# Kernel optimization log

Hardware: AMD Instinct MI355X
Metric: run time of the kernel (lower is better)

## Reference

```python
import jax, jax.numpy as jnp
import numpy as np

B, L, D_IN = 2048, 512, 32
PRED_LEN = 96
COND = 128      # cond_dim (z_dim)
XPROJ = 128     # x_proj_dim defaults to cond_dim
ODE_H = 128     # ode_hidden
TDIM = 128      # time_dim
HID = 256       # hidden of final MLP
N_STEPS = 32    # fixed-step RK4 steps over t in [0,1] (stands in for adaptive dopri5)
LN_EPS = 1e-5


def _linear(x, w, b):
    return x @ w.T + b


def _layernorm(x, g, b):
    mu = jnp.mean(x, axis=-1, keepdims=True)
    var = jnp.var(x, axis=-1, keepdims=True)
    return (x - mu) * jax.lax.rsqrt(var + LN_EPS) * g + b


def _interp(x_seq, t):
    # linear interp over sequence dim: x_seq (B,L,D), scalar t in [0,1] -> (B,D)
    Ls = x_seq.shape[1]
    pos = jnp.clip(t, 0.0, 1.0) * (Ls - 1)
    i0 = jnp.clip(jnp.floor(pos).astype(jnp.int32), 0, Ls - 1)
    i1 = jnp.clip(i0 + 1, 0, Ls - 1)
    w = (pos - i0.astype(pos.dtype))
    x0 = jax.lax.dynamic_index_in_dim(x_seq, i0, axis=1, keepdims=False)
    x1 = jax.lax.dynamic_index_in_dim(x_seq, i1, axis=1, keepdims=False)
    return (1.0 - w) * x0 + w * x1


def setup_inputs() -> dict:
    key = jax.random.key(0)
    ks = jax.random.split(key, 16)

    def kaiming(k, shape):
        return jax.random.normal(k, shape, jnp.float32) * np.float32(np.sqrt(2.0 / shape[-1]))

    IN_F = PRED_LEN * D_IN + COND + TDIM   # 3328
    OUT_F = PRED_LEN * D_IN                # 3072
    return {
        "x_t": jax.random.normal(ks[0], (B, PRED_LEN, D_IN), jnp.float32),
        "past": jax.random.normal(ks[1], (B, L, D_IN), jnp.float32),
        "t": jax.random.randint(ks[2], (B,), 0, 1000),
        "xproj_w": kaiming(ks[3], (XPROJ, D_IN)), "xproj_b": jnp.zeros((XPROJ,), jnp.float32),
        "z0_w": kaiming(ks[4], (COND, XPROJ)), "z0_b": jnp.zeros((COND,), jnp.float32),
        "ln_g": jnp.ones((COND,), jnp.float32), "ln_b": jnp.zeros((COND,), jnp.float32),
        "w1": kaiming(ks[5], (ODE_H, COND + XPROJ)), "b1": jnp.zeros((ODE_H,), jnp.float32),
        "w2": kaiming(ks[6], (ODE_H, ODE_H)), "b2": jnp.zeros((ODE_H,), jnp.float32),
        "w3": kaiming(ks[7], (COND, ODE_H)), "b3": jnp.zeros((COND,), jnp.float32),
        "fw1": kaiming(ks[8], (HID, IN_F)), "fb1": jnp.zeros((HID,), jnp.float32),
        "fw2": kaiming(ks[9], (HID, HID)), "fb2": jnp.zeros((HID,), jnp.float32),
        "fw3": kaiming(ks[10], (OUT_F, HID)), "fb3": jnp.zeros((OUT_F,), jnp.float32),
    }


def _time_emb(t):
    half = TDIM // 2
    freqs = jnp.exp(-np.float32(np.log(10000.0)) * jnp.arange(half, dtype=jnp.float32) / (half - 1))
    args = t.astype(jnp.float32)[:, None] * freqs[None, :]
    return jnp.concatenate([jnp.sin(args), jnp.cos(args)], axis=1)  # (B, TDIM)


def _forward(x_t, past, t, xproj_w, xproj_b, z0_w, z0_b, ln_g, ln_b,
             w1, b1, w2, b2, w3, b3, fw1, fb1, fw2, fb2, fw3, fb3):
    Bn = x_t.shape[0]
    x_seq = _linear(past, xproj_w, xproj_b)           # (B,L,XPROJ)
    z0 = _linear(x_seq[:, 0, :], z0_w, z0_b)          # (B,COND)

    def odef(tt, z):
        xt = _interp(x_seq, tt)                       # (B,XPROJ)
        zn = _layernorm(z, ln_g, ln_b)
        h = jnp.concatenate([zn, xt], axis=-1)
        h = jax.nn.silu(_linear(h, w1, b1))
        h = jax.nn.silu(_linear(h, w2, b2))
        return _linear(h, w3, b3)                     # (B,COND)

    dt = jnp.float32(1.0 / N_STEPS)

    def step(z, tt):
        k1 = odef(tt, z)
        k2 = odef(tt + dt * 0.5, z + dt * 0.5 * k1)
        k3 = odef(tt + dt * 0.5, z + dt * 0.5 * k2)
        k4 = odef(tt + dt, z + dt * k3)
        return z + (dt / 6.0) * (k1 + 2.0 * k2 + 2.0 * k3 + k4), None

    ts = jnp.arange(N_STEPS, dtype=jnp.float32) * dt
    cond, _ = jax.lax.scan(step, z0, ts)              # zT (B,COND)

    temb = _time_emb(t)                               # (B,TDIM)
    x_flat = x_t.reshape(Bn, -1)                      # (B,PRED_LEN*D_IN)
    h = jnp.concatenate([x_flat, cond, temb], axis=1)
    h = jax.nn.silu(_linear(h, fw1, fb1))
    h = jax.nn.silu(_linear(h, fw2, fb2))
    eps = _linear(h, fw3, fb3)
    return eps.reshape(Bn, PRED_LEN, D_IN)


def reference(x_t, past, t, xproj_w, xproj_b, z0_w, z0_b, ln_g, ln_b,
              w1, b1, w2, b2, w3, b3, fw1, fb1, fw2, fb2, fw3, fb3):
    return _forward(x_t, past, t, xproj_w, xproj_b, z0_w, z0_b, ln_g, ln_b,
                    w1, b1, w2, b2, w3, b3, fw1, fb1, fw2, fb2, fw3, fb3)
```

## Files before the change

### kernel.cpp

```cpp
#include <hip/hip_runtime.h>
#include <math.h>

typedef _Float16 h8f16 __attribute__((ext_vector_type(8)));
typedef _Float16 h2f16 __attribute__((ext_vector_type(2)));
typedef float f32x4 __attribute__((ext_vector_type(4)));

#define MFMA16(a, b, c) __builtin_amdgcn_mfma_f32_16x16x32_f16((a), (b), (c), 0, 0, 0)

__device__ __forceinline__ float silu_f(float v) {
    return v * __builtin_amdgcn_rcpf(1.0f + __expf(-v));
}

__device__ __forceinline__ void bar_lds() {
    asm volatile("s_waitcnt lgkmcnt(0)" ::: "memory");
    __builtin_amdgcn_s_barrier();
    __builtin_amdgcn_sched_barrier(0);
}

__global__ __launch_bounds__(512, 1) void ode_kernel(
    const float* __restrict__ past,
    const float* __restrict__ xproj_w, const float* __restrict__ xproj_b,
    const float* __restrict__ z0_w, const float* __restrict__ z0_b,
    const float* __restrict__ ln_g, const float* __restrict__ ln_b,
    const float* __restrict__ w1, const float* __restrict__ b1,
    const float* __restrict__ w2, const float* __restrict__ b2,
    const float* __restrict__ w3, const float* __restrict__ b3,
    float* __restrict__ zbuf)
{
    __shared__ _Float16 hbuf[16][136];
    __shared__ _Float16 h1S[16][136];
    __shared__ _Float16 h2S[16][136];
    __shared__ float    pS[16][33];
    __shared__ float    x0S[16][128];
    __shared__ float    zS0[16][129];

    const int tid  = threadIdx.x;
    const int wid  = tid >> 6;
    const int lane = tid & 63;
    const int lrow = lane & 15;
    const int lhi  = lane >> 4;
    const int b0   = blockIdx.x * 16;
    const int nc   = wid * 16 + lrow;
    const int koff = lhi * 8;

    h8f16 w1f[4], wcf, w2f[4], w3f[4];
    float b1t, b2r, b3r;
    {
#pragma unroll
        for (int ks = 0; ks < 4; ++ks) {
            h8f16 v1, v2, v3;
#pragma unroll
            for (int j = 0; j < 8; ++j) {
                const int k = ks * 32 + koff + j;
                v1[j] = (_Float16)(w1[nc * 256 + k] * ln_g[k]);
                v2[j] = (_Float16)w2[nc * 128 + k];
                v3[j] = (_Float16)w3[nc * 128 + k];
            }
            w1f[ks] = v1; w2f[ks] = v2; w3f[ks] = v3;
        }
        float wc[8] = {0, 0, 0, 0, 0, 0, 0, 0};
        float bc = 0.0f, bb = 0.0f;
        const float* w1a = w1 + nc * 256;
        const float* w1b = w1a + 128;
#pragma unroll 4
        for (int k = 0; k < 128; ++k) {
            const float a = w1b[k];
            bc += a * xproj_b[k];
            bb += w1a[k] * ln_b[k];
            const float* xr = xproj_w + k * 32 + koff;
#pragma unroll
            for (int j = 0; j < 8; ++j) wc[j] += a * xr[j];
        }
        h8f16 v;
#pragma unroll
        for (int j = 0; j < 8; ++j) v[j] = (_Float16)wc[j];
        wcf = v;
        b1t = b1[nc] + bc + bb;
        b2r = b2[nc]; b3r = b3[nc];
    }

    pS[tid >> 5][tid & 31] = past[(long)(b0 + (tid >> 5)) * 16384 + (tid & 31)];
    __syncthreads();
    {
        const int r  = tid >> 5;
        const int c0 = (tid & 31) * 4;
#pragma unroll
        for (int cc = 0; cc < 4; ++cc) {
            const int kc = c0 + cc;
            float s = xproj_b[kc];
            const float* xr = xproj_w + kc * 32;
#pragma unroll
            for (int c = 0; c < 32; ++c) s += pS[r][c] * xr[c];
            x0S[r][kc] = s;
        }
    }
    __syncthreads();
    {
        const int nn = tid & 127;
        const int r0 = (tid >> 7) * 4;
        for (int p = 0; p < 4; ++p) {
            const int r = r0 + p;
            float s = z0_b[nn];
            const float* zr = z0_w + nn * 128;
            for (int k = 0; k < 128; ++k) s += x0S[r][k] * zr[k];
            zS0[r][nn] = s;
        }
    }
    __syncthreads();

    float zc[4], krk[4];
#pragma unroll
    for (int j = 0; j < 4; ++j) {
        zc[j] = zS0[4 * lhi + j][nc];
        hbuf[4 * lhi + j][nc] = (_Float16)zc[j];
    }

    const float DT = 1.0f / 32.0f;

    f32x4 s0a, s0b, s1a, s1b;
    auto stage = [&](int e) {
        const float pos = (float)e * 7.984375f;
        const int i0 = (int)pos;
        const int i1 = (i0 < 511) ? i0 + 1 : 511;
        const float* base = past + (long)(b0 + lrow) * 16384;
        const float* p0 = base + i0 * 32 + koff;
        const float* p1 = base + i1 * 32 + koff;
        s0a = *(const f32x4*)p0; s0b = *(const f32x4*)(p0 + 4);
        s1a = *(const f32x4*)p1; s1b = *(const f32x4*)(p1 + 4);
    };
    auto blend = [&](int e) -> h8f16 {
        const float pos = (float)e * 7.984375f;
        const float w = pos - floorf(pos);
        h8f16 r;
#pragma unroll
        for (int j = 0; j < 4; ++j) {
            r[j]     = (_Float16)(s0a[j] + w * (s1a[j] - s0a[j]));
            r[4 + j] = (_Float16)(s0b[j] + w * (s1b[j] - s0b[j]));
        }
        return r;
    };

    const h2f16 one2 = {(_Float16)1.0f, (_Float16)1.0f};

    auto phaseA = [&](h8f16 bxc) {
        h8f16 xf[4];
#pragma unroll
        for (int ks = 0; ks < 4; ++ks)
            xf[ks] = *(const h8f16*)&hbuf[lrow][ks * 32 + koff];
        float s0 = 0.f, s1 = 0.f, q0 = 0.f, q1 = 0.f;
#pragma unroll
        for (int ks = 0; ks < 4; ++ks) {
#pragma unroll
            for (int p = 0; p < 4; ++p) {
                const h2f16 x2 = {xf[ks][2 * p], xf[ks][2 * p + 1]};
                if (p & 1) {
                    s1 = __builtin_amdgcn_fdot2(x2, one2, s1, false);
                    q1 = __builtin_amdgcn_fdot2(x2, x2, q1, false);
                } else {
                    s0 = __builtin_amdgcn_fdot2(x2, one2, s0, false);
                    q0 = __builtin_amdgcn_fdot2(x2, x2, q0, false);
                }
            }
        }
        float s = s0 + s1, q = q0 + q1;
        s += __shfl_xor(s, 16); q += __shfl_xor(q, 16);
        s += __shfl_xor(s, 32); q += __shfl_xor(q, 32);
        const float mu  = s * (1.0f / 128.0f);
        const float var = q * (1.0f / 128.0f) - mu * mu;
        const float inv = 1.0f / sqrtf(var + 1e-5f);
        const _Float16 ih = (_Float16)inv;
        const _Float16 mh = (_Float16)(-mu * inv);
        h8f16 ip, mp;
#pragma unroll
        for (int j = 0; j < 8; ++j) { ip[j] = ih; mp[j] = mh; }
        f32x4 acc = {0, 0, 0, 0};
#pragma unroll
        for (int ks = 0; ks < 4; ++ks) {
            const h8f16 az = xf[ks] * ip + mp;
            acc = MFMA16(az, w1f[ks], acc);
        }
        acc = MFMA16(bxc, wcf, acc);
#pragma unroll
        for (int j = 0; j < 4; ++j)
            h1S[4 * lhi + j][nc] = (_Float16)silu_f(acc[j] + b1t);
    };
    auto phaseB = [&]() {
        f32x4 acc = {0, 0, 0, 0};
#pragma unroll
        for (int ks = 0; ks < 4; ++ks) {
            const h8f16 a = *(const h8f16*)&h1S[lrow][ks * 32 + koff];
            acc = MFMA16(a, w2f[ks], acc);
        }
#pragma unroll
        for (int j = 0; j < 4; ++j)
            h2S[4 * lhi + j][nc] = (_Float16)silu_f(acc[j] + b2r);
    };
    auto phaseC = [&]() -> f32x4 {
        f32x4 acc = {0, 0, 0, 0};
#pragma unroll
        for (int ks = 0; ks < 4; ++ks) {
            const h8f16 a = *(const h8f16*)&h2S[lrow][ks * 32 + koff];
            acc = MFMA16(a, w3f[ks], acc);
        }
#pragma unroll
        for (int j = 0; j < 4; ++j) acc[j] += b3r;
        return acc;
    };

    stage(0);
    h8f16 bxc = blend(0);
    __syncthreads();

#pragma unroll 1
    for (int st = 0; st < 32; ++st) {
        const int e1 = 2 * st + 1, e2 = 2 * st + 2;
        phaseA(bxc);
        stage(e1);
        bar_lds();
        phaseB(); bar_lds();
        {
            const f32x4 k = phaseC();
#pragma unroll
            for (int j = 0; j < 4; ++j) {
                krk[j] = k[j];
                hbuf[4 * lhi + j][nc] = (_Float16)(zc[j] + 0.5f * DT * k[j]);
            }
        }
        bar_lds();
        bxc = blend(e1);
        phaseA(bxc); bar_lds();
        phaseB(); bar_lds();
        {
            const f32x4 k = phaseC();
#pragma unroll
            for (int j = 0; j < 4; ++j) {
                krk[j] += 2.0f * k[j];
                hbuf[4 * lhi + j][nc] = (_Float16)(zc[j] + 0.5f * DT * k[j]);
            }
        }
        bar_lds();
        phaseA(bxc);
        stage(e2);
        bar_lds();
        phaseB(); bar_lds();
        {
            const f32x4 k = phaseC();
#pragma unroll
            for (int j = 0; j < 4; ++j) {
                krk[j] += 2.0f * k[j];
                hbuf[4 * lhi + j][nc] = (_Float16)(zc[j] + DT * k[j]);
            }
        }
        bar_lds();
        bxc = blend(e2);
        phaseA(bxc); bar_lds();
        phaseB(); bar_lds();
        {
            const f32x4 k = phaseC();
#pragma unroll
            for (int j = 0; j < 4; ++j) {
                zc[j] += (DT / 6.0f) * (krk[j] + k[j]);
                hbuf[4 * lhi + j][nc] = (_Float16)zc[j];
            }
        }
        bar_lds();
    }

#pragma unroll
    for (int j = 0; j < 4; ++j)
        zbuf[(long)(b0 + 4 * lhi + j) * 128 + nc] = zc[j];
}

__global__ __launch_bounds__(256) void hcat_kernel(
    const float* __restrict__ x_t, const float* __restrict__ cond,
    const int* __restrict__ tvals, _Float16* __restrict__ hcat)
{
    const int gid = blockIdx.x * 256 + threadIdx.x;
    const int b  = gid / 416;
    const int j0 = (gid % 416) * 8;
    h8f16 v;
    if (j0 < 3072) {
        const float* s = x_t + (long)b * 3072 + j0;
#pragma unroll
        for (int j = 0; j < 8; ++j) v[j] = (_Float16)s[j];
    } else if (j0 < 3200) {
        const float* s = cond + (long)b * 128 + (j0 - 3072);
#pragma unroll
        for (int j = 0; j < 8; ++j) v[j] = (_Float16)s[j];
    } else {
        const float tv = (float)tvals[b];
#pragma unroll
        for (int j = 0; j < 8; ++j) {
            const int jj  = j0 - 3200 + j;
            const int idx = (jj < 64) ? jj : jj - 64;
            const float fr = expf(-9.210340371976184f * (float)idx * (1.0f / 63.0f));
            const float a  = tv * fr;
            v[j] = (_Float16)((jj < 64) ? sinf(a) : cosf(a));
        }
    }
    *(h8f16*)&hcat[(long)b * 3328 + j0] = v;
}

template <bool SILU, bool OUT_F16>
__global__ __launch_bounds__(256) void gemm_f16(
    const _Float16* __restrict__ A, const float* __restrict__ W,
    const float* __restrict__ bias, void* __restrict__ out,
    int M, int N, int K)
{
    __shared__ _Float16 aS[64][40];
    __shared__ _Float16 wS[64][40];
    const int mb = blockIdx.x * 64, nb = blockIdx.y * 64;
    const int tid = threadIdx.x, lane = tid & 63, wq = tid >> 6;
    const int lrow = lane & 15, lhi = lane >> 4;
    f32x4 acc[4];
#pragma unroll
    for (int nt = 0; nt < 4; ++nt) acc[nt] = (f32x4){0, 0, 0, 0};

    const int sr = tid >> 2;
    const int sk = (tid & 3) * 8;

    for (int k0 = 0; k0 < K; k0 += 32) {
        {
            h8f16 v = *(const h8f16*)&A[(long)(mb + sr) * K + k0 + sk];
            *(h8f16*)&aS[sr][sk] = v;
        }
        {
            const float* s = &W[(long)(nb + sr) * K + k0 + sk];
            h8f16 v;
#pragma unroll
            for (int j = 0; j < 8; ++j) v[j] = (_Float16)s[j];
            *(h8f16*)&wS[sr][sk] = v;
        }
        __syncthreads();
        h8f16 a = *(const h8f16*)&aS[wq * 16 + lrow][lhi * 8];
#pragma unroll
        for (int nt = 0; nt < 4; ++nt) {
            h8f16 bfr = *(const h8f16*)&wS[nt * 16 + lrow][lhi * 8];
            acc[nt] = MFMA16(a, bfr, acc[nt]);
        }
        __syncthreads();
    }

#pragma unroll
    for (int nt = 0; nt < 4; ++nt) {
        const int cc = nb + nt * 16 + lrow;
        const float bv = bias[cc];
#pragma unroll
        for (int j = 0; j < 4; ++j) {
            const int rr = mb + wq * 16 + lhi * 4 + j;
            float v = acc[nt][j] + bv;
            if (SILU) v = silu_f(v);
            if (OUT_F16) ((_Float16*)out)[(long)rr * N + cc] = (_Float16)v;
            else         ((float*)out)[(long)rr * N + cc] = v;
        }
    }
}

extern "C" void kernel_launch(void* const* d_in, const int* in_sizes, int n_in,
                              void* d_out, int out_size, void* d_ws, size_t ws_size,
                              hipStream_t stream)
{
    const float* x_t     = (const float*)d_in[0];
    const float* past    = (const float*)d_in[1];
    const int*   tvals   = (const int*)d_in[2];
    const float* xproj_w = (const float*)d_in[3];
    const float* xproj_b = (const float*)d_in[4];
    const float* z0_w    = (const float*)d_in[5];
    const float* z0_b    = (const float*)d_in[6];
    const float* ln_g    = (const float*)d_in[7];
    const float* ln_b    = (const float*)d_in[8];
    const float* w1      = (const float*)d_in[9];
    const float* b1      = (const float*)d_in[10];
    const float* w2      = (const float*)d_in[11];
    const float* b2      = (const float*)d_in[12];
    const float* w3      = (const float*)d_in[13];
    const float* b3      = (const float*)d_in[14];
    const float* fw1     = (const float*)d_in[15];
    const float* fb1     = (const float*)d_in[16];
    const float* fw2     = (const float*)d_in[17];
    const float* fb2     = (const float*)d_in[18];
    const float* fw3     = (const float*)d_in[19];
    const float* fb3     = (const float*)d_in[20];

    char* ws = (char*)d_ws;
    float*     zbuf = (float*)ws;
    _Float16*  hcat = (_Float16*)(ws + (1 << 20));
    _Float16*  h1   = (_Float16*)(ws + 15 * (1 << 20));
    _Float16*  h2   = (_Float16*)(ws + 16 * (1 << 20));

    ode_kernel<<<128, 512, 0, stream>>>(past, xproj_w, xproj_b, z0_w, z0_b,
                                        ln_g, ln_b, w1, b1, w2, b2, w3, b3, zbuf);

    hcat_kernel<<<(2048 * 416) / 256, 256, 0, stream>>>(x_t, zbuf, tvals, hcat);

    gemm_f16<true,  true ><<<dim3(32, 4),  256, 0, stream>>>(hcat, fw1, fb1, h1, 2048, 256, 3328);
    gemm_f16<true,  true ><<<dim3(32, 4),  256, 0, stream>>>(h1,   fw2, fb2, h2, 2048, 256, 256);
    gemm_f16<false, false><<<dim3(32, 48), 256, 0, stream>>>(h2,   fw3, fb3, d_out, 2048, 3072, 256);
}
```

Before: 324.3 us.

## Halve ODE block waves, precompute interpolated inputs into LDS, permute weight K-layout

The ODE kernel now runs 4 waves per block instead of 8, and each wave computes two 16-column output tiles. Weight columns are permuted so each lane writes two adjacent fp16 outputs with one packed store. All 65 interpolated past inputs are precomputed into a large LDS table up front, so the RK4 loop no longer does global loads. The loop also becomes a compact sub-step loop. This reduces barrier participants and in-loop memory latency, at the cost of more registers per wave, half as many waves for latency hiding, and an upfront staging phase.

```diff
diff --git a/kernel.cpp b/kernel.cpp
--- a/kernel.cpp
+++ b/kernel.cpp
@@ -2,6 +2,7 @@
 #include <math.h>
 
 typedef _Float16 h8f16 __attribute__((ext_vector_type(8)));
+typedef _Float16 h4f16 __attribute__((ext_vector_type(4)));
 typedef _Float16 h2f16 __attribute__((ext_vector_type(2)));
 typedef float f32x4 __attribute__((ext_vector_type(4)));
 
@@ -17,7 +18,7 @@
     __builtin_amdgcn_sched_barrier(0);
 }
 
-__global__ __launch_bounds__(512, 1) void ode_kernel(
+__global__ __launch_bounds__(256, 1) void ode_kernel(
     const float* __restrict__ past,
     const float* __restrict__ xproj_w, const float* __restrict__ xproj_b,
     const float* __restrict__ z0_w, const float* __restrict__ z0_b,
@@ -27,6 +28,7 @@
     const float* __restrict__ w3, const float* __restrict__ b3,
     float* __restrict__ zbuf)
 {
+    __shared__ _Float16 bxAll[65][16][40];
     __shared__ _Float16 hbuf[16][136];
     __shared__ _Float16 h1S[16][136];
     __shared__ _Float16 h2S[16][136];
@@ -35,32 +37,38 @@
     __shared__ float    zS0[16][129];
 
     const int tid  = threadIdx.x;
-    const int wid  = tid >> 6;
+    const int wq   = tid >> 6;
     const int lane = tid & 63;
     const int lrow = lane & 15;
     const int lhi  = lane >> 4;
     const int b0   = blockIdx.x * 16;
-    const int nc   = wid * 16 + lrow;
     const int koff = lhi * 8;
 
-    h8f16 w1f[4], wcf, w2f[4], w3f[4];
-    float b1t, b2r, b3r;
-    {
+    const int PERM[8] = {0, 16, 1, 17, 2, 18, 3, 19};
+
+    h8f16 w1f[2][4], wcf[2], w2f[2][4], w3f[2][4];
+    float b1t[2], b2r[2], b3r[2];
+#pragma unroll
+    for (int nt = 0; nt < 2; ++nt) {
+        const int n = wq * 32 + nt * 16 + lrow;
 #pragma unroll
         for (int ks = 0; ks < 4; ++ks) {
+            const float* s1 = w1 + n * 256 + ks * 32 + lhi * 4;
+            const float* g1 = ln_g + ks * 32 + lhi * 4;
+            const float* s2 = w2 + n * 128 + ks * 32 + lhi * 4;
+            const float* s3 = w3 + n * 128 + ks * 32 + lhi * 4;
             h8f16 v1, v2, v3;
 #pragma unroll
             for (int j = 0; j < 8; ++j) {
-                const int k = ks * 32 + koff + j;
-                v1[j] = (_Float16)(w1[nc * 256 + k] * ln_g[k]);
-                v2[j] = (_Float16)w2[nc * 128 + k];
-                v3[j] = (_Float16)w3[nc * 128 + k];
+                v1[j] = (_Float16)(s1[PERM[j]] * g1[PERM[j]]);
+                v2[j] = (_Float16)s2[PERM[j]];
+                v3[j] = (_Float16)s3[PERM[j]];
             }
-            w1f[ks] = v1; w2f[ks] = v2; w3f[ks] = v3;
+            w1f[nt][ks] = v1; w2f[nt][ks] = v2; w3f[nt][ks] = v3;
         }
         float wc[8] = {0, 0, 0, 0, 0, 0, 0, 0};
         float bc = 0.0f, bb = 0.0f;
-        const float* w1a = w1 + nc * 256;
+        const float* w1a = w1 + n * 256;
         const float* w1b = w1a + 128;
 #pragma unroll 4
         for (int k = 0; k < 128; ++k) {
@@ -74,18 +82,19 @@
         h8f16 v;
 #pragma unroll
         for (int j = 0; j < 8; ++j) v[j] = (_Float16)wc[j];
-        wcf = v;
-        b1t = b1[nc] + bc + bb;
-        b2r = b2[nc]; b3r = b3[nc];
-    }
-
-    pS[tid >> 5][tid & 31] = past[(long)(b0 + (tid >> 5)) * 16384 + (tid & 31)];
+        wcf[nt] = v;
+        b1t[nt] = b1[n] + bc + bb;
+        b2r[nt] = b2[n]; b3r[nt] = b3[n];
+    }
+
+    for (int i = tid; i < 512; i += 256)
+        pS[i >> 5][i & 31] = past[(long)(b0 + (i >> 5)) * 16384 + (i & 31)];
     __syncthreads();
     {
-        const int r  = tid >> 5;
-        const int c0 = (tid & 31) * 4;
-#pragma unroll
-        for (int cc = 0; cc < 4; ++cc) {
+        const int r  = tid >> 4;
+        const int c0 = (tid & 15) * 8;
+#pragma unroll
+        for (int cc = 0; cc < 8; ++cc) {
             const int kc = c0 + cc;
             float s = xproj_b[kc];
             const float* xr = xproj_w + kc * 32;
@@ -97,8 +106,8 @@
     __syncthreads();
     {
         const int nn = tid & 127;
-        const int r0 = (tid >> 7) * 4;
-        for (int p = 0; p < 4; ++p) {
+        const int r0 = (tid >> 7) * 8;
+        for (int p = 0; p < 8; ++p) {
             const int r = r0 + p;
             float s = z0_b[nn];
             const float* zr = z0_w + nn * 128;
@@ -106,43 +115,41 @@
             zS0[r][nn] = s;
         }
     }
-    __syncthreads();
-
-    float zc[4], krk[4];
-#pragma unroll
-    for (int j = 0; j < 4; ++j) {
-        zc[j] = zS0[4 * lhi + j][nc];
-        hbuf[4 * lhi + j][nc] = (_Float16)zc[j];
-    }
-
-    const float DT = 1.0f / 32.0f;
-
-    f32x4 s0a, s0b, s1a, s1b;
-    auto stage = [&](int e) {
+
+    for (int flat = tid; flat < 65 * 128; flat += 256) {
+        const int e  = flat >> 7;
+        const int u  = flat & 127;
+        const int r  = u >> 3;
+        const int c  = (u & 7) * 4;
         const float pos = (float)e * 7.984375f;
         const int i0 = (int)pos;
         const int i1 = (i0 < 511) ? i0 + 1 : 511;
-        const float* base = past + (long)(b0 + lrow) * 16384;
-        const float* p0 = base + i0 * 32 + koff;
-        const float* p1 = base + i1 * 32 + koff;
-        s0a = *(const f32x4*)p0; s0b = *(const f32x4*)(p0 + 4);
-        s1a = *(const f32x4*)p1; s1b = *(const f32x4*)(p1 + 4);
-    };
-    auto blend = [&](int e) -> h8f16 {
-        const float pos = (float)e * 7.984375f;
-        const float w = pos - floorf(pos);
-        h8f16 r;
-#pragma unroll
-        for (int j = 0; j < 4; ++j) {
-            r[j]     = (_Float16)(s0a[j] + w * (s1a[j] - s0a[j]));
-            r[4 + j] = (_Float16)(s0b[j] + w * (s1b[j] - s0b[j]));
-        }
-        return r;
-    };
-
+        const float w = pos - (float)i0;
+        const f32x4 a0 = *(const f32x4*)(past + ((long)(b0 + r) * 512 + i0) * 32 + c);
+        const f32x4 a1 = *(const f32x4*)(past + ((long)(b0 + r) * 512 + i1) * 32 + c);
+        h4f16 v;
+#pragma unroll
+        for (int j = 0; j < 4; ++j) v[j] = (_Float16)((1.0f - w) * a0[j] + w * a1[j]);
+        *(h4f16*)&bxAll[e][r][c] = v;
+    }
+    __syncthreads();
+
+    const int cA = wq * 32 + lrow, cB = cA + 16;
+    const int pc = wq * 32 + 2 * lrow;
+    float zc[2][4];
+#pragma unroll
+    for (int j = 0; j < 4; ++j) {
+        zc[0][j] = zS0[4 * lhi + j][cA];
+        zc[1][j] = zS0[4 * lhi + j][cB];
+        *(h2f16*)&hbuf[4 * lhi + j][pc] = (h2f16){(_Float16)zc[0][j], (_Float16)zc[1][j]};
+    }
+
+    f32x4 krk[2];
+    krk[0] = (f32x4){0, 0, 0, 0}; krk[1] = (f32x4){0, 0, 0, 0};
+    const float DT = 1.0f / 32.0f;
     const h2f16 one2 = {(_Float16)1.0f, (_Float16)1.0f};
 
-    auto phaseA = [&](h8f16 bxc) {
+    auto phaseA = [&](int e) {
         h8f16 xf[4];
 #pragma unroll
         for (int ks = 0; ks < 4; ++ks)
@@ -173,102 +180,90 @@
         h8f16 ip, mp;
 #pragma unroll
         for (int j = 0; j < 8; ++j) { ip[j] = ih; mp[j] = mh; }
-        f32x4 acc = {0, 0, 0, 0};
+        const h8f16 bx = *(const h8f16*)&bxAll[e][lrow][koff];
+        f32x4 a0 = {0, 0, 0, 0}, a1 = {0, 0, 0, 0};
 #pragma unroll
         for (int ks = 0; ks < 4; ++ks) {
             const h8f16 az = xf[ks] * ip + mp;
-            acc = MFMA16(az, w1f[ks], acc);
-        }
-        acc = MFMA16(bxc, wcf, acc);
-#pragma unroll
-        for (int j = 0; j < 4; ++j)
-            h1S[4 * lhi + j][nc] = (_Float16)silu_f(acc[j] + b1t);
+            a0 = MFMA16(az, w1f[0][ks], a0);
+            a1 = MFMA16(az, w1f[1][ks], a1);
+        }
+        a0 = MFMA16(bx, wcf[0], a0);
+        a1 = MFMA16(bx, wcf[1], a1);
+#pragma unroll
+        for (int j = 0; j < 4; ++j) {
+            const _Float16 o0 = (_Float16)silu_f(a0[j] + b1t[0]);
+            const _Float16 o1 = (_Float16)silu_f(a1[j] + b1t[1]);
+            *(h2f16*)&h1S[4 * lhi + j][pc] = (h2f16){o0, o1};
+        }
     };
     auto phaseB = [&]() {
-        f32x4 acc = {0, 0, 0, 0};
+        f32x4 a0 = {0, 0, 0, 0}, a1 = {0, 0, 0, 0};
 #pragma unroll
         for (int ks = 0; ks < 4; ++ks) {
             const h8f16 a = *(const h8f16*)&h1S[lrow][ks * 32 + koff];
-            acc = MFMA16(a, w2f[ks], acc);
-        }
-#pragma unroll
-        for (int j = 0; j < 4; ++j)
-            h2S[4 * lhi + j][nc] = (_Float16)silu_f(acc[j] + b2r);
+            a0 = MFMA16(a, w2f[0][ks], a0);
+            a1 = MFMA16(a, w2f[1][ks], a1);
+        }
+#pragma unroll
+        for (int j = 0; j < 4; ++j) {
+            const _Float16 o0 = (_Float16)silu_f(a0[j] + b2r[0]);
+            const _Float16 o1 = (_Float16)silu_f(a1[j] + b2r[1]);
+            *(h2f16*)&h2S[4 * lhi + j][pc] = (h2f16){o0, o1};
+        }
     };
-    auto phaseC = [&]() -> f32x4 {
-        f32x4 acc = {0, 0, 0, 0};
-#pragma unroll
-        for (int ks = 0; ks < 4; ++ks) {
-            const h8f16 a = *(const h8f16*)&h2S[lrow][ks * 32 + koff];
-            acc = MFMA16(a, w3f[ks], acc);
-        }
-#pragma unroll
-        for (int j = 0; j < 4; ++j) acc[j] += b3r;
-        return acc;
-    };
-
-    stage(0);
-    h8f16 bxc = blend(0);
-    __syncthreads();
 
 #pragma unroll 1
-    for (int st = 0; st < 32; ++st) {
-        const int e1 = 2 * st + 1, e2 = 2 * st + 2;
-        phaseA(bxc);
-        stage(e1);
-        bar_lds();
-        phaseB(); bar_lds();
-        {
-            const f32x4 k = phaseC();
-#pragma unroll
-            for (int j = 0; j < 4; ++j) {
-                krk[j] = k[j];
-                hbuf[4 * lhi + j][nc] = (_Float16)(zc[j] + 0.5f * DT * k[j]);
+    for (int step = 0; step < 32; ++step) {
+#pragma unroll 1
+        for (int sub = 0; sub < 4; ++sub) {
+            const int e = 2 * step + ((sub + 1) >> 1);
+            phaseA(e);  bar_lds();
+            phaseB();   bar_lds();
+            {
+                f32x4 a0 = {0, 0, 0, 0}, a1 = {0, 0, 0, 0};
+#pragma unroll
+                for (int ks = 0; ks < 4; ++ks) {
+                    const h8f16 a = *(const h8f16*)&h2S[lrow][ks * 32 + koff];
+                    a0 = MFMA16(a, w3f[0][ks], a0);
+                    a1 = MFMA16(a, w3f[1][ks], a1);
+                }
+#pragma unroll
+                for (int j = 0; j < 4; ++j) {
+                    const float k0v = a0[j] + b3r[0];
+                    const float k1v = a1[j] + b3r[1];
+                    float v0, v1;
+                    if (sub == 0) {
+                        krk[0][j] = k0v; krk[1][j] = k1v;
+                        v0 = zc[0][j] + 0.5f * DT * k0v;
+                        v1 = zc[1][j] + 0.5f * DT * k1v;
+                    } else if (sub == 1) {
+                        krk[0][j] += 2.0f * k0v; krk[1][j] += 2.0f * k1v;
+                        v0 = zc[0][j] + 0.5f * DT * k0v;
+                        v1 = zc[1][j] + 0.5f * DT * k1v;
+                    } else if (sub == 2) {
+                        krk[0][j] += 2.0f * k0v; krk[1][j] += 2.0f * k1v;
+                        v0 = zc[0][j] + DT * k0v;
+                        v1 = zc[1][j] + DT * k1v;
+                    } else {
+                        zc[0][j] += (DT / 6.0f) * (krk[0][j] + k0v);
+                        zc[1][j] += (DT / 6.0f) * (krk[1][j] + k1v);
+                        v0 = zc[0][j];
+                        v1 = zc[1][j];
+                    }
+                    *(h2f16*)&hbuf[4 * lhi + j][pc] = (h2f16){(_Float16)v0, (_Float16)v1};
+                }
             }
-        }
-        bar_lds();
-        bxc = blend(e1);
-        phaseA(bxc); bar_lds();
-        phaseB(); bar_lds();
-        {
-            const f32x4 k = phaseC();
-#pragma unroll
-            for (int j = 0; j < 4; ++j) {
-                krk[j] += 2.0f * k[j];
-                hbuf[4 * lhi + j][nc] = (_Float16)(zc[j] + 0.5f * DT * k[j]);
-            }
-        }
-        bar_lds();
-        phaseA(bxc);
-        stage(e2);
-        bar_lds();
-        phaseB(); bar_lds();
-        {
-            const f32x4 k = phaseC();
-#pragma unroll
-            for (int j = 0; j < 4; ++j) {
-                krk[j] += 2.0f * k[j];
-                hbuf[4 * lhi + j][nc] = (_Float16)(zc[j] + DT * k[j]);
-            }
-        }
-        bar_lds();
-        bxc = blend(e2);
-        phaseA(bxc); bar_lds();
-        phaseB(); bar_lds();
-        {
-            const f32x4 k = phaseC();
-#pragma unroll
-            for (int j = 0; j < 4; ++j) {
-                zc[j] += (DT / 6.0f) * (krk[j] + k[j]);
-                hbuf[4 * lhi + j][nc] = (_Float16)zc[j];
-            }
-        }
-        bar_lds();
-    }
-
-#pragma unroll
-    for (int j = 0; j < 4; ++j)
-        zbuf[(long)(b0 + 4 * lhi + j) * 128 + nc] = zc[j];
+            bar_lds();
+        }
+    }
+
+#pragma unroll
+    for (int j = 0; j < 4; ++j) {
+        const long rb = (long)(b0 + 4 * lhi + j) * 128;
+        zbuf[rb + cA] = zc[0][j];
+        zbuf[rb + cB] = zc[1][j];
+    }
 }
 
 __global__ __launch_bounds__(256) void hcat_kernel(
@@ -388,7 +383,7 @@
     _Float16*  h1   = (_Float16*)(ws + 15 * (1 << 20));
     _Float16*  h2   = (_Float16*)(ws + 16 * (1 << 20));
 
-    ode_kernel<<<128, 512, 0, stream>>>(past, xproj_w, xproj_b, z0_w, z0_b,
+    ode_kernel<<<128, 256, 0, stream>>>(past, xproj_w, xproj_b, z0_w, z0_b,
                                         ln_g, ln_b, w1, b1, w2, b2, w3, b3, zbuf);
 
     hcat_kernel<<<(2048 * 416) / 256, 256, 0, stream>>>(x_t, zbuf, tvals, hcat);
```

New measurement: 370.5 us. 1.14x slower.

## Process two independent 16-row batch tiles per ODE block to interleave chains

Applied to the files above, without the earlier changes.

Each ODE workgroup now handles 32 batch rows as two independent 16-row tiles (A and B), with separate LDS buffers and register state. Every RK4 stage issues the MFMA/LayerNorm/SiLU phases for both tiles between the same barriers. The grid shrinks from 128 to 64 blocks. The aim is to fill the latency-bound serial chain with independent work and to pay fewer barriers per row, at the cost of using half as many CUs and more registers and LDS per block.

```diff
diff --git a/kernel.cpp b/kernel.cpp
--- a/kernel.cpp
+++ b/kernel.cpp
@@ -27,19 +27,18 @@
     const float* __restrict__ w3, const float* __restrict__ b3,
     float* __restrict__ zbuf)
 {
-    __shared__ _Float16 hbuf[16][136];
-    __shared__ _Float16 h1S[16][136];
-    __shared__ _Float16 h2S[16][136];
-    __shared__ float    pS[16][33];
-    __shared__ float    x0S[16][128];
-    __shared__ float    zS0[16][129];
+    __shared__ _Float16 hbA[16][136], h1A[16][136], h2A[16][136];
+    __shared__ _Float16 hbB[16][136], h1B[16][136], h2B[16][136];
+    __shared__ float    pS[32][33];
+    __shared__ float    x0S[32][128];
+    __shared__ float    zS0[32][129];
 
     const int tid  = threadIdx.x;
     const int wid  = tid >> 6;
     const int lane = tid & 63;
     const int lrow = lane & 15;
     const int lhi  = lane >> 4;
-    const int b0   = blockIdx.x * 16;
+    const int b0   = blockIdx.x * 32;
     const int nc   = wid * 16 + lrow;
     const int koff = lhi * 8;
 
@@ -79,13 +78,14 @@
         b2r = b2[nc]; b3r = b3[nc];
     }
 
-    pS[tid >> 5][tid & 31] = past[(long)(b0 + (tid >> 5)) * 16384 + (tid & 31)];
+    for (int i = tid; i < 32 * 32; i += 512)
+        pS[i >> 5][i & 31] = past[(long)(b0 + (i >> 5)) * 16384 + (i & 31)];
     __syncthreads();
     {
-        const int r  = tid >> 5;
-        const int c0 = (tid & 31) * 4;
-#pragma unroll
-        for (int cc = 0; cc < 4; ++cc) {
+        const int r  = tid >> 4;
+        const int c0 = (tid & 15) * 8;
+#pragma unroll
+        for (int cc = 0; cc < 8; ++cc) {
             const int kc = c0 + cc;
             float s = xproj_b[kc];
             const float* xr = xproj_w + kc * 32;
@@ -97,8 +97,8 @@
     __syncthreads();
     {
         const int nn = tid & 127;
-        const int r0 = (tid >> 7) * 4;
-        for (int p = 0; p < 4; ++p) {
+        const int r0 = (tid >> 7) * 8;
+        for (int p = 0; p < 8; ++p) {
             const int r = r0 + p;
             float s = z0_b[nn];
             const float* zr = z0_w + nn * 128;
@@ -108,45 +108,68 @@
     }
     __syncthreads();
 
-    float zc[4], krk[4];
+    float zcA[4], krkA[4], zcB[4], krkB[4];
 #pragma unroll
     for (int j = 0; j < 4; ++j) {
-        zc[j] = zS0[4 * lhi + j][nc];
-        hbuf[4 * lhi + j][nc] = (_Float16)zc[j];
+        zcA[j] = zS0[4 * lhi + j][nc];
+        zcB[j] = zS0[16 + 4 * lhi + j][nc];
+        hbA[4 * lhi + j][nc] = (_Float16)zcA[j];
+        hbB[4 * lhi + j][nc] = (_Float16)zcB[j];
     }
 
     const float DT = 1.0f / 32.0f;
-
-    f32x4 s0a, s0b, s1a, s1b;
-    auto stage = [&](int e) {
+    const h2f16 one2 = {(_Float16)1.0f, (_Float16)1.0f};
+
+    f32x4 sA0a, sA0b, sA1a, sA1b;
+    f32x4 sB0a, sB0b, sB1a, sB1b;
+    auto stageA = [&](int e) {
         const float pos = (float)e * 7.984375f;
         const int i0 = (int)pos;
         const int i1 = (i0 < 511) ? i0 + 1 : 511;
         const float* base = past + (long)(b0 + lrow) * 16384;
         const float* p0 = base + i0 * 32 + koff;
         const float* p1 = base + i1 * 32 + koff;
-        s0a = *(const f32x4*)p0; s0b = *(const f32x4*)(p0 + 4);
-        s1a = *(const f32x4*)p1; s1b = *(const f32x4*)(p1 + 4);
-    };
-    auto blend = [&](int e) -> h8f16 {
+        sA0a = *(const f32x4*)p0; sA0b = *(const f32x4*)(p0 + 4);
+        sA1a = *(const f32x4*)p1; sA1b = *(const f32x4*)(p1 + 4);
+    };
+    auto stageB = [&](int e) {
+        const float pos = (float)e * 7.984375f;
+        const int i0 = (int)pos;
+        const int i1 = (i0 < 511) ? i0 + 1 : 511;
+        const float* base = past + (long)(b0 + 16 + lrow) * 16384;
+        const float* p0 = base + i0 * 32 + koff;
+        const float* p1 = base + i1 * 32 + koff;
+        sB0a = *(const f32x4*)p0; sB0b = *(const f32x4*)(p0 + 4);
+        sB1a = *(const f32x4*)p1; sB1b = *(const f32x4*)(p1 + 4);
+    };
+    auto blendA = [&](int e) -> h8f16 {
         const float pos = (float)e * 7.984375f;
         const float w = pos - floorf(pos);
         h8f16 r;
 #pragma unroll
         for (int j = 0; j < 4; ++j) {
-            r[j]     = (_Float16)(s0a[j] + w * (s1a[j] - s0a[j]));
-            r[4 + j] = (_Float16)(s0b[j] + w * (s1b[j] - s0b[j]));
+            r[j]     = (_Float16)(sA0a[j] + w * (sA1a[j] - sA0a[j]));
+            r[4 + j] = (_Float16)(sA0b[j] + w * (sA1b[j] - sA0b[j]));
         }
         return r;
     };
-
-    const h2f16 one2 = {(_Float16)1.0f, (_Float16)1.0f};
-
-    auto phaseA = [&](h8f16 bxc) {
+    auto blendB = [&](int e) -> h8f16 {
+        const float pos = (float)e * 7.984375f;
+        const float w = pos - floorf(pos);
+        h8f16 r;
+#pragma unroll
+        for (int j = 0; j < 4; ++j) {
+            r[j]     = (_Float16)(sB0a[j] + w * (sB1a[j] - sB0a[j]));
+            r[4 + j] = (_Float16)(sB0b[j] + w * (sB1b[j] - sB0b[j]));
+        }
+        return r;
+    };
+
+    auto phaseA = [&](const _Float16 (*hb)[136], _Float16 (*h1)[136], h8f16 bx) {
         h8f16 xf[4];
 #pragma unroll
         for (int ks = 0; ks < 4; ++ks)
-            xf[ks] = *(const h8f16*)&hbuf[lrow][ks * 32 + koff];
+            xf[ks] = *(const h8f16*)&hb[lrow][ks * 32 + koff];
         float s0 = 0.f, s1 = 0.f, q0 = 0.f, q1 = 0.f;
 #pragma unroll
         for (int ks = 0; ks < 4; ++ks) {
@@ -179,27 +202,27 @@
             const h8f16 az = xf[ks] * ip + mp;
             acc = MFMA16(az, w1f[ks], acc);
         }
-        acc = MFMA16(bxc, wcf, acc);
+        acc = MFMA16(bx, wcf, acc);
 #pragma unroll
         for (int j = 0; j < 4; ++j)
-            h1S[4 * lhi + j][nc] = (_Float16)silu_f(acc[j] + b1t);
-    };
-    auto phaseB = [&]() {
+            h1[4 * lhi + j][nc] = (_Float16)silu_f(acc[j] + b1t);
+    };
+    auto phaseB = [&](const _Float16 (*h1)[136], _Float16 (*h2)[136]) {
         f32x4 acc = {0, 0, 0, 0};
 #pragma unroll
         for (int ks = 0; ks < 4; ++ks) {
-            const h8f16 a = *(const h8f16*)&h1S[lrow][ks * 32 + koff];
+            const h8f16 a = *(const h8f16*)&h1[lrow][ks * 32 + koff];
             acc = MFMA16(a, w2f[ks], acc);
         }
 #pragma unroll
         for (int j = 0; j < 4; ++j)
-            h2S[4 * lhi + j][nc] = (_Float16)silu_f(acc[j] + b2r);
-    };
-    auto phaseC = [&]() -> f32x4 {
+            h2[4 * lhi + j][nc] = (_Float16)silu_f(acc[j] + b2r);
+    };
+    auto phaseC = [&](const _Float16 (*h2)[136]) -> f32x4 {
         f32x4 acc = {0, 0, 0, 0};
 #pragma unroll
         for (int ks = 0; ks < 4; ++ks) {
-            const h8f16 a = *(const h8f16*)&h2S[lrow][ks * 32 + koff];
+            const h8f16 a = *(const h8f16*)&h2[lrow][ks * 32 + koff];
             acc = MFMA16(a, w3f[ks], acc);
         }
 #pragma unroll
@@ -207,68 +230,83 @@
         return acc;
     };
 
-    stage(0);
-    h8f16 bxc = blend(0);
+    stageA(0); stageB(0);
+    h8f16 bxcA = blendA(0);
+    h8f16 bxcB = blendB(0);
     __syncthreads();
 
 #pragma unroll 1
     for (int st = 0; st < 32; ++st) {
         const int e1 = 2 * st + 1, e2 = 2 * st + 2;
-        phaseA(bxc);
-        stage(e1);
-        bar_lds();
-        phaseB(); bar_lds();
-        {
-            const f32x4 k = phaseC();
+        phaseA(hbA, h1A, bxcA); phaseA(hbB, h1B, bxcB);
+        stageA(e1); stageB(e1);
+        bar_lds();
+        phaseB(h1A, h2A); phaseB(h1B, h2B); bar_lds();
+        {
+            const f32x4 kA = phaseC(h2A);
+            const f32x4 kB = phaseC(h2B);
 #pragma unroll
             for (int j = 0; j < 4; ++j) {
-                krk[j] = k[j];
-                hbuf[4 * lhi + j][nc] = (_Float16)(zc[j] + 0.5f * DT * k[j]);
-            }
-        }
-        bar_lds();
-        bxc = blend(e1);
-        phaseA(bxc); bar_lds();
-        phaseB(); bar_lds();
-        {
-            const f32x4 k = phaseC();
+                krkA[j] = kA[j];
+                krkB[j] = kB[j];
+                hbA[4 * lhi + j][nc] = (_Float16)(zcA[j] + 0.5f * DT * kA[j]);
+                hbB[4 * lhi + j][nc] = (_Float16)(zcB[j] + 0.5f * DT * kB[j]);
+            }
+        }
+        bar_lds();
+        bxcA = blendA(e1); bxcB = blendB(e1);
+        phaseA(hbA, h1A, bxcA); phaseA(hbB, h1B, bxcB); bar_lds();
+        phaseB(h1A, h2A); phaseB(h1B, h2B); bar_lds();
+        {
+            const f32x4 kA = phaseC(h2A);
+            const f32x4 kB = phaseC(h2B);
 #pragma unroll
             for (int j = 0; j < 4; ++j) {
-                krk[j] += 2.0f * k[j];
-                hbuf[4 * lhi + j][nc] = (_Float16)(zc[j] + 0.5f * DT * k[j]);
-            }
-        }
-        bar_lds();
-        phaseA(bxc);
-        stage(e2);
-        bar_lds();
-        phaseB(); bar_lds();
-        {
-            const f32x4 k = phaseC();
+                krkA[j] += 2.0f * kA[j];
+                krkB[j] += 2.0f * kB[j];
+                hbA[4 * lhi + j][nc] = (_Float16)(zcA[j] + 0.5f * DT * kA[j]);
+                hbB[4 * lhi + j][nc] = (_Float16)(zcB[j] + 0.5f * DT * kB[j]);
+            }
+        }
+        bar_lds();
+        phaseA(hbA, h1A, bxcA); phaseA(hbB, h1B, bxcB);
+        stageA(e2); stageB(e2);
+        bar_lds();
+        phaseB(h1A, h2A); phaseB(h1B, h2B); bar_lds();
+        {
+            const f32x4 kA = phaseC(h2A);
+            const f32x4 kB = phaseC(h2B);
 #pragma unroll
             for (int j = 0; j < 4; ++j) {
-                krk[j] += 2.0f * k[j];
-                hbuf[4 * lhi + j][nc] = (_Float16)(zc[j] + DT * k[j]);
-            }
-        }
-        bar_lds();
-        bxc = blend(e2);
-        phaseA(bxc); bar_lds();
-        phaseB(); bar_lds();
-        {
-            const f32x4 k = phaseC();
+                krkA[j] += 2.0f * kA[j];
+                krkB[j] += 2.0f * kB[j];
+                hbA[4 * lhi + j][nc] = (_Float16)(zcA[j] + DT * kA[j]);
+                hbB[4 * lhi + j][nc] = (_Float16)(zcB[j] + DT * kB[j]);
+            }
+        }
+        bar_lds();
+        bxcA = blendA(e2); bxcB = blendB(e2);
+        phaseA(hbA, h1A, bxcA); phaseA(hbB, h1B, bxcB); bar_lds();
+        phaseB(h1A, h2A); phaseB(h1B, h2B); bar_lds();
+        {
+            const f32x4 kA = phaseC(h2A);
+            const f32x4 kB = phaseC(h2B);
 #pragma unroll
             for (int j = 0; j < 4; ++j) {
-                zc[j] += (DT / 6.0f) * (krk[j] + k[j]);
-                hbuf[4 * lhi + j][nc] = (_Float16)zc[j];
-            }
-        }
-        bar_lds();
-    }
-
-#pragma unroll
-    for (int j = 0; j < 4; ++j)
-        zbuf[(long)(b0 + 4 * lhi + j) * 128 + nc] = zc[j];
+                zcA[j] += (DT / 6.0f) * (krkA[j] + kA[j]);
+                zcB[j] += (DT / 6.0f) * (krkB[j] + kB[j]);
+                hbA[4 * lhi + j][nc] = (_Float16)zcA[j];
+                hbB[4 * lhi + j][nc] = (_Float16)zcB[j];
+            }
+        }
+        bar_lds();
+    }
+
+#pragma unroll
+    for (int j = 0; j < 4; ++j) {
+        zbuf[(long)(b0 + 4 * lhi + j) * 128 + nc]      = zcA[j];
+        zbuf[(long)(b0 + 16 + 4 * lhi + j) * 128 + nc] = zcB[j];
+    }
 }
 
 __global__ __launch_bounds__(256) void hcat_kernel(
@@ -388,8 +426,8 @@
     _Float16*  h1   = (_Float16*)(ws + 15 * (1 << 20));
     _Float16*  h2   = (_Float16*)(ws + 16 * (1 << 20));
 
-    ode_kernel<<<128, 512, 0, stream>>>(past, xproj_w, xproj_b, z0_w, z0_b,
-                                        ln_g, ln_b, w1, b1, w2, b2, w3, b3, zbuf);
+    ode_kernel<<<64, 512, 0, stream>>>(past, xproj_w, xproj_b, z0_w, z0_b,
+                                       ln_g, ln_b, w1, b1, w2, b2, w3, b3, zbuf);
 
     hcat_kernel<<<(2048 * 416) / 256, 256, 0, stream>>>(x_t, zbuf, tvals, hcat);
 
```

After: 525.1 us. +61.9%, slower.

## Overlap x_t part of first MLP GEMM and time embedding with ODE blocks

Applied to the files above, without the earlier changes.

The first MLP layer is split by K. The large x_t slice (K=3072) and the sinusoidal time embedding no longer depend on the ODE result, so they are computed by extra blocks launched in the same grid as the 128 ODE blocks and run concurrently on idle CUs. A small follow-up GEMM handles the cond and temb columns (K=256), adds the precomputed partial sums, bias and SiLU. This removes the separate hcat concat kernel and its fp16 round trip, and hides most of the big GEMM behind the latency-bound ODE integration. In exchange it writes an fp32 partial-sum buffer, and the overlap relies on enough CUs being free.

```diff
diff --git a/kernel.cpp b/kernel.cpp
--- a/kernel.cpp
+++ b/kernel.cpp
@@ -2,6 +2,7 @@
 #include <math.h>
 
 typedef _Float16 h8f16 __attribute__((ext_vector_type(8)));
+typedef _Float16 h4f16 __attribute__((ext_vector_type(4)));
 typedef _Float16 h2f16 __attribute__((ext_vector_type(2)));
 typedef float f32x4 __attribute__((ext_vector_type(4)));
 
@@ -17,7 +18,7 @@
     __builtin_amdgcn_sched_barrier(0);
 }
 
-__global__ __launch_bounds__(512, 1) void ode_kernel(
+__global__ __launch_bounds__(512, 1) void fat_kernel(
     const float* __restrict__ past,
     const float* __restrict__ xproj_w, const float* __restrict__ xproj_b,
     const float* __restrict__ z0_w, const float* __restrict__ z0_b,
@@ -25,16 +26,108 @@
     const float* __restrict__ w1, const float* __restrict__ b1,
     const float* __restrict__ w2, const float* __restrict__ b2,
     const float* __restrict__ w3, const float* __restrict__ b3,
-    float* __restrict__ zbuf)
+    const float* __restrict__ x_t, const float* __restrict__ fw1,
+    const int* __restrict__ tvals,
+    float* __restrict__ zbuf, float* __restrict__ h1pre,
+    _Float16* __restrict__ tbuf)
 {
-    __shared__ _Float16 hbuf[16][136];
-    __shared__ _Float16 h1S[16][136];
-    __shared__ _Float16 h2S[16][136];
-    __shared__ float    pS[16][33];
-    __shared__ float    x0S[16][128];
-    __shared__ float    zS0[16][129];
-
-    const int tid  = threadIdx.x;
+    __shared__ union {
+        struct {
+            _Float16 hbuf[16][136];
+            _Float16 h1S[16][136];
+            _Float16 h2S[16][136];
+            float    pS[16][33];
+            float    x0S[16][128];
+            float    zS0[16][129];
+        } ode;
+        struct {
+            _Float16 aS[128][40];
+            _Float16 wS[64][40];
+        } gx;
+    } sm;
+
+    const int tid = threadIdx.x;
+
+    if (blockIdx.x >= 192) {
+        const int t = blockIdx.x - 192;
+        for (int c = 0; c < 8; ++c) {
+            const int chunk = t * 512 + tid + c * 4096;
+            const int b  = chunk >> 4;
+            const int j0 = (chunk & 15) * 8;
+            const float tv = (float)tvals[b];
+            h8f16 v;
+#pragma unroll
+            for (int j = 0; j < 8; ++j) {
+                const int jj  = j0 + j;
+                const int idx = (jj < 64) ? jj : jj - 64;
+                const float fr = expf(-9.210340371976184f * (float)idx * (1.0f / 63.0f));
+                const float a  = tv * fr;
+                v[j] = (_Float16)((jj < 64) ? sinf(a) : cosf(a));
+            }
+            *(h8f16*)&tbuf[(long)b * 128 + j0] = v;
+        }
+        return;
+    }
+
+    if (blockIdx.x >= 128) {
+        const int g  = blockIdx.x - 128;
+        const int mb = (g >> 2) * 128;
+        const int nb = (g & 3) * 64;
+        const int lane = tid & 63, wid = tid >> 6;
+        const int lrow = lane & 15, lhi = lane >> 4;
+        f32x4 acc[4];
+#pragma unroll
+        for (int nt = 0; nt < 4; ++nt) acc[nt] = (f32x4){0, 0, 0, 0};
+
+        const int sra = tid >> 2, ska = (tid & 3) * 8;
+        const int srw = tid >> 3, skw = (tid & 7) * 4;
+
+        for (int k0 = 0; k0 < 3072; k0 += 32) {
+            {
+                const float* s = x_t + (long)(mb + sra) * 3072 + k0 + ska;
+                const f32x4 u0 = *(const f32x4*)s;
+                const f32x4 u1 = *(const f32x4*)(s + 4);
+                h8f16 v;
+#pragma unroll
+                for (int j = 0; j < 4; ++j) { v[j] = (_Float16)u0[j]; v[4 + j] = (_Float16)u1[j]; }
+                *(h8f16*)&sm.gx.aS[sra][ska] = v;
+            }
+            {
+                const float* s = fw1 + (long)(nb + srw) * 3328 + k0 + skw;
+                const f32x4 u = *(const f32x4*)s;
+                h4f16 v;
+#pragma unroll
+                for (int j = 0; j < 4; ++j) v[j] = (_Float16)u[j];
+                *(h4f16*)&sm.gx.wS[srw][skw] = v;
+            }
+            __syncthreads();
+            const h8f16 a = *(const h8f16*)&sm.gx.aS[wid * 16 + lrow][lhi * 8];
+#pragma unroll
+            for (int nt = 0; nt < 4; ++nt) {
+                const h8f16 bfr = *(const h8f16*)&sm.gx.wS[nt * 16 + lrow][lhi * 8];
+                acc[nt] = MFMA16(a, bfr, acc[nt]);
+            }
+            __syncthreads();
+        }
+#pragma unroll
+        for (int nt = 0; nt < 4; ++nt) {
+            const int cc = nb + nt * 16 + lrow;
+#pragma unroll
+            for (int j = 0; j < 4; ++j) {
+                const int rr = mb + wid * 16 + lhi * 4 + j;
+                h1pre[(long)rr * 256 + cc] = acc[nt][j];
+            }
+        }
+        return;
+    }
+
+    _Float16 (&hbuf)[16][136] = sm.ode.hbuf;
+    _Float16 (&h1S)[16][136]  = sm.ode.h1S;
+    _Float16 (&h2S)[16][136]  = sm.ode.h2S;
+    float    (&pS)[16][33]    = sm.ode.pS;
+    float    (&x0S)[16][128]  = sm.ode.x0S;
+    float    (&zS0)[16][129]  = sm.ode.zS0;
+
     const int wid  = tid >> 6;
     const int lane = tid & 63;
     const int lrow = lane & 15;
@@ -79,7 +172,9 @@
         b2r = b2[nc]; b3r = b3[nc];
     }
 
-    pS[tid >> 5][tid & 31] = past[(long)(b0 + (tid >> 5)) * 16384 + (tid & 31)];
+    if (tid < 512) {
+        pS[tid >> 5][tid & 31] = past[(long)(b0 + (tid >> 5)) * 16384 + (tid & 31)];
+    }
     __syncthreads();
     {
         const int r  = tid >> 5;
@@ -271,34 +366,64 @@
         zbuf[(long)(b0 + 4 * lhi + j) * 128 + nc] = zc[j];
 }
 
-__global__ __launch_bounds__(256) void hcat_kernel(
-    const float* __restrict__ x_t, const float* __restrict__ cond,
-    const int* __restrict__ tvals, _Float16* __restrict__ hcat)
+__global__ __launch_bounds__(256) void gemm1c_kernel(
+    const float* __restrict__ cond, const _Float16* __restrict__ tbuf,
+    const float* __restrict__ fw1, const float* __restrict__ fb1,
+    const float* __restrict__ h1pre, _Float16* __restrict__ h1)
 {
-    const int gid = blockIdx.x * 256 + threadIdx.x;
-    const int b  = gid / 416;
-    const int j0 = (gid % 416) * 8;
-    h8f16 v;
-    if (j0 < 3072) {
-        const float* s = x_t + (long)b * 3072 + j0;
-#pragma unroll
-        for (int j = 0; j < 8; ++j) v[j] = (_Float16)s[j];
-    } else if (j0 < 3200) {
-        const float* s = cond + (long)b * 128 + (j0 - 3072);
-#pragma unroll
-        for (int j = 0; j < 8; ++j) v[j] = (_Float16)s[j];
-    } else {
-        const float tv = (float)tvals[b];
-#pragma unroll
-        for (int j = 0; j < 8; ++j) {
-            const int jj  = j0 - 3200 + j;
-            const int idx = (jj < 64) ? jj : jj - 64;
-            const float fr = expf(-9.210340371976184f * (float)idx * (1.0f / 63.0f));
-            const float a  = tv * fr;
-            v[j] = (_Float16)((jj < 64) ? sinf(a) : cosf(a));
-        }
-    }
-    *(h8f16*)&hcat[(long)b * 3328 + j0] = v;
+    __shared__ _Float16 aS[64][40];
+    __shared__ _Float16 wS[64][40];
+    const int mb = blockIdx.x * 64, nb = blockIdx.y * 64;
+    const int tid = threadIdx.x, lane = tid & 63, wq = tid >> 6;
+    const int lrow = lane & 15, lhi = lane >> 4;
+    f32x4 acc[4];
+#pragma unroll
+    for (int nt = 0; nt < 4; ++nt) acc[nt] = (f32x4){0, 0, 0, 0};
+
+    const int sr = tid >> 2;
+    const int sk = (tid & 3) * 8;
+
+    for (int k0 = 0; k0 < 256; k0 += 32) {
+        if (k0 < 128) {
+            const float* s = cond + (long)(mb + sr) * 128 + k0 + sk;
+            const f32x4 u0 = *(const f32x4*)s;
+            const f32x4 u1 = *(const f32x4*)(s + 4);
+            h8f16 v;
+#pragma unroll
+            for (int j = 0; j < 4; ++j) { v[j] = (_Float16)u0[j]; v[4 + j] = (_Float16)u1[j]; }
+            *(h8f16*)&aS[sr][sk] = v;
+        } else {
+            *(h8f16*)&aS[sr][sk] =
+                *(const h8f16*)&tbuf[(long)(mb + sr) * 128 + (k0 - 128) + sk];
+        }
+        {
+            const float* s = fw1 + (long)(nb + sr) * 3328 + 3072 + k0 + sk;
+            h8f16 v;
+#pragma unroll
+            for (int j = 0; j < 8; ++j) v[j] = (_Float16)s[j];
+            *(h8f16*)&wS[sr][sk] = v;
+        }
+        __syncthreads();
+        const h8f16 a = *(const h8f16*)&aS[wq * 16 + lrow][lhi * 8];
+#pragma unroll
+        for (int nt = 0; nt < 4; ++nt) {
+            const h8f16 bfr = *(const h8f16*)&wS[nt * 16 + lrow][lhi * 8];
+            acc[nt] = MFMA16(a, bfr, acc[nt]);
+        }
+        __syncthreads();
+    }
+
+#pragma unroll
+    for (int nt = 0; nt < 4; ++nt) {
+        const int cc = nb + nt * 16 + lrow;
+        const float bv = fb1[cc];
+#pragma unroll
+        for (int j = 0; j < 4; ++j) {
+            const int rr = mb + wq * 16 + lhi * 4 + j;
+            const float v = acc[nt][j] + h1pre[(long)rr * 256 + cc] + bv;
+            h1[(long)rr * 256 + cc] = (_Float16)silu_f(v);
+        }
+    }
 }
 
 template <bool SILU, bool OUT_F16>
@@ -383,17 +508,18 @@
     const float* fb3     = (const float*)d_in[20];
 
     char* ws = (char*)d_ws;
-    float*     zbuf = (float*)ws;
-    _Float16*  hcat = (_Float16*)(ws + (1 << 20));
-    _Float16*  h1   = (_Float16*)(ws + 15 * (1 << 20));
-    _Float16*  h2   = (_Float16*)(ws + 16 * (1 << 20));
-
-    ode_kernel<<<128, 512, 0, stream>>>(past, xproj_w, xproj_b, z0_w, z0_b,
-                                        ln_g, ln_b, w1, b1, w2, b2, w3, b3, zbuf);
-
-    hcat_kernel<<<(2048 * 416) / 256, 256, 0, stream>>>(x_t, zbuf, tvals, hcat);
-
-    gemm_f16<true,  true ><<<dim3(32, 4),  256, 0, stream>>>(hcat, fw1, fb1, h1, 2048, 256, 3328);
-    gemm_f16<true,  true ><<<dim3(32, 4),  256, 0, stream>>>(h1,   fw2, fb2, h2, 2048, 256, 256);
-    gemm_f16<false, false><<<dim3(32, 48), 256, 0, stream>>>(h2,   fw3, fb3, d_out, 2048, 3072, 256);
+    float*     zbuf  = (float*)ws;
+    _Float16*  tbuf  = (_Float16*)(ws + (1 << 20));
+    float*     h1pre = (float*)(ws + 2 * (1 << 20));
+    _Float16*  h1    = (_Float16*)(ws + 4 * (1 << 20));
+    _Float16*  h2    = (_Float16*)(ws + 5 * (1 << 20));
+
+    fat_kernel<<<200, 512, 0, stream>>>(past, xproj_w, xproj_b, z0_w, z0_b,
+                                        ln_g, ln_b, w1, b1, w2, b2, w3, b3,
+                                        x_t, fw1, tvals, zbuf, h1pre, tbuf);
+
+    gemm1c_kernel<<<dim3(32, 4), 256, 0, stream>>>(zbuf, tbuf, fw1, fb1, h1pre, h1);
+
+    gemm_f16<true,  true ><<<dim3(32, 4),  256, 0, stream>>>(h1, fw2, fb2, h2, 2048, 256, 256);
+    gemm_f16<false, false><<<dim3(32, 48), 256, 0, stream>>>(h2, fw3, fb3, d_out, 2048, 3072, 256);
 }
```

New measurement: 368.6 us. +13.7%, slower.
